# Performance work log

Measured on AMD Instinct MI355X. Metric: run time of the kernel, lower is better.

Reference implementation:

```python
import jax, jax.numpy as jnp
import numpy as np

B, T, I, H, O = 64, 2048, 128, 256, 128
K1 = 1
K2 = 1


def setup_inputs() -> dict:
    key = jax.random.key(0)
    ks = jax.random.split(key, 8)
    M = H - K1 + 1
    return {
        "x": jax.random.normal(ks[0], (B, T, I), jnp.float32),
        "W_in": jax.random.normal(ks[1], (H, I), jnp.float32) / np.sqrt(I).astype(np.float32),
        "b_in": jax.random.normal(ks[2], (H,), jnp.float32) * 0.01,
        "W_out": jax.random.normal(ks[3], (O, H), jnp.float32) / np.sqrt(H).astype(np.float32),
        "b_out": jax.random.normal(ks[4], (O,), jnp.float32) * 0.01,
        # padded Householder vectors: row i uses its first K+i entries (masked in reference)
        # uniform in [0.5, 1.5] keeps u.u well away from 0 (avoids 2/<u,u> blowup)
        "u_raw": jax.random.uniform(ks[5], (M, H), jnp.float32, 0.5, 1.5),
        "sigmas": jnp.ones((H,), jnp.float32),
        "v_raw": jax.random.uniform(ks[6], (M, H), jnp.float32, 0.5, 1.5),
    }


def _householder_chain(hats):
    # U <- H_last @ ... @ H_0, H_i = I - 2/<u,u> u u^T, applied as rank-1 updates
    Hdim = hats.shape[1]
    def step(Umat, u):
        beta = 2.0 / jnp.dot(u, u)
        return Umat - beta * jnp.outer(u, u @ Umat), None
    U, _ = jax.lax.scan(step, jnp.eye(Hdim, dtype=hats.dtype), hats)
    return U


def reference(x, W_in, b_in, W_out, b_out, u_raw, sigmas, v_raw):
    Hdim = sigmas.shape[0]
    Mu = u_raw.shape[0]
    Mv = v_raw.shape[0]
    # row i of u_hats has entries in cols [0, K1+i), then flipped along cols
    mask_u = jnp.arange(Hdim)[None, :] < (K1 + jnp.arange(Mu))[:, None]
    u_hats = jnp.flip(jnp.where(mask_u, u_raw, 0.0), axis=1)
    mask_v = jnp.arange(Hdim)[None, :] < (K2 + jnp.arange(Mv))[:, None]
    v_hats = jnp.flip(jnp.where(mask_v, v_raw, 0.0), axis=(0, 1))  # torch.flip dims=[0,1]
    U = _householder_chain(u_hats)
    V = _householder_chain(v_hats)
    W = (U * sigmas[None, :]) @ V  # U @ diag(sigmas) @ V
    # precompute input projection for all timesteps: [T, B, H]
    xproj = jnp.einsum('bti,hi->tbh', x, W_in) + b_in
    h0 = jnp.zeros((x.shape[0], Hdim), x.dtype)
    def cell(h, xp):
        h = jnp.tanh(xp + h @ W.T)
        return h, h @ W_out.T + b_out
    _, out = jax.lax.scan(cell, h0, xproj)  # out: [T, B, O]
    return jnp.transpose(out, (1, 0, 2))
```

## Files before the change

kernel.cpp:

```cpp
#include <hip/hip_runtime.h>
#include <hip/hip_bf16.h>
#include <hip/hip_fp16.h>

#define BB 64
#define TT 2048
#define II 128
#define HH 256
#define OO 128
#define RCH 8

typedef _Float16 f16x2 __attribute__((ext_vector_type(2)));
typedef _Float16 f16x8 __attribute__((ext_vector_type(8)));
typedef float f32x4 __attribute__((ext_vector_type(4)));

#if __has_builtin(__builtin_amdgcn_fdot2)
__device__ __forceinline__ float fdot2(f16x2 a, f16x2 b, float c) {
    return __builtin_amdgcn_fdot2(a, b, c, false);
}
#else
__device__ __forceinline__ float fdot2(f16x2 a, f16x2 b, float c) {
    return fmaf((float)a.x, (float)b.x, fmaf((float)a.y, (float)b.y, c));
}
#endif

__device__ __forceinline__ f16x2 u2h(unsigned int u) { return __builtin_bit_cast(f16x2, u); }
__device__ __forceinline__ unsigned int packf16(float a, float b) {
    return __builtin_bit_cast(unsigned int, f16x2{(_Float16)a, (_Float16)b});
}

__device__ __forceinline__ float tanh_fast(float x) {
    float xc = fminf(fmaxf(x, -9.0f), 9.0f);
    float e = __expf(2.0f * xc);
    return (e - 1.0f) * __fdividef(1.0f, e + 1.0f);
}

__device__ __forceinline__ void step_barrier() {
    __builtin_amdgcn_sched_barrier(0);
    asm volatile("s_waitcnt lgkmcnt(0)" ::: "memory");
    __builtin_amdgcn_s_barrier();
    __builtin_amdgcn_sched_barrier(0);
}

__global__ __launch_bounds__(64) void prep_kernel(
    const float* __restrict__ u_raw, const float* __restrict__ v_raw,
    float* __restrict__ u_eff, float* __restrict__ v_eff,
    float* __restrict__ beta_u, float* __restrict__ beta_v)
{
    const int row = blockIdx.x;
    const int lane = threadIdx.x;
    const bool isU = row < HH;
    const int i = isU ? row : row - HH;
    const float* src = isU ? (u_raw + (size_t)i * HH) : (v_raw + (size_t)(HH - 1 - i) * HH);
    float* dst = (isU ? u_eff : v_eff) + (size_t)i * HH;
    const int lo = isU ? (HH - 1 - i) : i;
    float ss = 0.0f;
    for (int c = lane; c < HH; c += 64) {
        float vv = (c >= lo) ? src[HH - 1 - c] : 0.0f;
        dst[c] = vv;
        ss += vv * vv;
    }
    for (int m = 1; m < 64; m <<= 1) ss += __shfl_xor(ss, m, 64);
    if (lane == 0) (isU ? beta_u : beta_v)[i] = 2.0f / ss;
}

__global__ __launch_bounds__(256) void hh_kernel(
    const float* __restrict__ u_eff, const float* __restrict__ v_eff,
    const float* __restrict__ beta_u, const float* __restrict__ beta_v,
    float* __restrict__ Ucol, float* __restrict__ Vrow)
{
    const int wid = blockIdx.x * 4 + (threadIdx.x >> 6);
    const int lane = threadIdx.x & 63;
    const bool isU = wid < HH;
    const int j = isU ? wid : wid - HH;
    const float* eff = isU ? u_eff : v_eff;
    const float* beta = isU ? beta_u : beta_v;

    float cr0 = (j == 4 * lane + 0) ? 1.0f : 0.0f;
    float cr1 = (j == 4 * lane + 1) ? 1.0f : 0.0f;
    float cr2 = (j == 4 * lane + 2) ? 1.0f : 0.0f;
    float cr3 = (j == 4 * lane + 3) ? 1.0f : 0.0f;

    const int i0 = isU ? (HH - 1 - j) : 0;
    for (int i = i0; i < HH; ++i) {
        const float4 v4 = *(const float4*)(eff + (size_t)i * HH + lane * 4);
        float d = v4.x * cr0 + v4.y * cr1 + v4.z * cr2 + v4.w * cr3;
        for (int m = 1; m < 64; m <<= 1) d += __shfl_xor(d, m, 64);
        const float t = beta[i] * d;
        cr0 = fmaf(-t, v4.x, cr0);
        cr1 = fmaf(-t, v4.y, cr1);
        cr2 = fmaf(-t, v4.z, cr2);
        cr3 = fmaf(-t, v4.w, cr3);
    }
    if (isU) {
        *(float4*)(Ucol + (size_t)j * HH + lane * 4) = make_float4(cr0, cr1, cr2, cr3);
    } else {
        Vrow[(size_t)(4 * lane + 0) * HH + j] = cr0;
        Vrow[(size_t)(4 * lane + 1) * HH + j] = cr1;
        Vrow[(size_t)(4 * lane + 2) * HH + j] = cr2;
        Vrow[(size_t)(4 * lane + 3) * HH + j] = cr3;
    }
}

__global__ __launch_bounds__(256) void w_kernel(
    const float* __restrict__ Ucol, const float* __restrict__ Vrow,
    const float* __restrict__ sig, float* __restrict__ Wm)
{
    const int r = blockIdx.x;
    const int c = threadIdx.x;
    float acc = 0.0f;
    #pragma unroll 4
    for (int k = 0; k < HH; ++k) {
        acc = fmaf(Ucol[(size_t)k * HH + r] * sig[k], Vrow[(size_t)k * HH + c], acc);
    }
    Wm[(size_t)r * HH + c] = acc;
}

__device__ __forceinline__ void stage16(_Float16* dst, const float* src) {
    #pragma unroll
    for (int i = 0; i < 4; ++i) {
        float4 f = ((const float4*)src)[i];
        ((f16x2*)dst)[2 * i + 0] = f16x2{(_Float16)f.x, (_Float16)f.y};
        ((f16x2*)dst)[2 * i + 1] = f16x2{(_Float16)f.z, (_Float16)f.w};
    }
}
__device__ __forceinline__ void stage16(_Float16* dst, const __half* src) {
    ((uint4*)dst)[0] = ((const uint4*)src)[0];
    ((uint4*)dst)[1] = ((const uint4*)src)[1];
}
__device__ __forceinline__ void storeC(float* p, float v) { *p = v; }
__device__ __forceinline__ void storeC(__half* p, float v) { *p = __float2half_rn(v); }

template <typename AT, typename OT>
__global__ __launch_bounds__(256) void gemm_mfma(
    const AT* __restrict__ A, const float* __restrict__ Bm,
    const float* __restrict__ bias, OT* __restrict__ C,
    int M, int N, int K)
{
    __shared__ _Float16 As[128][40];
    __shared__ _Float16 Bs[64][40];
    const int tid = threadIdx.x;
    const int m0 = blockIdx.x * 128;
    const int n0 = blockIdx.y * 64;
    const int lane = tid & 63;
    const int w = tid >> 6;
    const int lo = lane & 15;
    const int qd = lane >> 4;
    const int mh = w >> 1;
    const int nh = w & 1;
    const int srow = tid >> 1;
    const int shalf = tid & 1;

    f32x4 acc[4][2] = {};
    for (int k0 = 0; k0 < K; k0 += 32) {
        stage16(&As[srow][shalf * 16], A + (size_t)(m0 + srow) * K + k0 + shalf * 16);
        if (tid < 128)
            stage16(&Bs[srow][shalf * 16], Bm + (size_t)(n0 + srow) * K + k0 + shalf * 16);
        __syncthreads();
        f16x8 af[4], bf[2];
        #pragma unroll
        for (int mt = 0; mt < 4; ++mt)
            af[mt] = *(const f16x8*)&As[64 * mh + 16 * mt + lo][qd * 8];
        #pragma unroll
        for (int nt = 0; nt < 2; ++nt)
            bf[nt] = *(const f16x8*)&Bs[32 * nh + 16 * nt + lo][qd * 8];
        #pragma unroll
        for (int mt = 0; mt < 4; ++mt)
            #pragma unroll
            for (int nt = 0; nt < 2; ++nt)
                acc[mt][nt] = __builtin_amdgcn_mfma_f32_16x16x32_f16(
                    af[mt], bf[nt], acc[mt][nt], 0, 0, 0);
        __syncthreads();
    }
    #pragma unroll
    for (int nt = 0; nt < 2; ++nt) {
        const int n = n0 + 32 * nh + 16 * nt + lo;
        const float bv = bias[n];
        #pragma unroll
        for (int mt = 0; mt < 4; ++mt) {
            const int m = m0 + 64 * mh + 16 * mt + 4 * qd;
            #pragma unroll
            for (int r = 0; r < 4; ++r)
                storeC(C + (size_t)(m + r) * N + n, acc[mt][nt][r] + bv);
        }
    }
}

__global__ __launch_bounds__(512) void recur_kernel(
    const float* __restrict__ Wm,
    const __half* __restrict__ xp,
    __half* __restrict__ hall)
{
    const int b = blockIdx.x;
    const int tid = threadIdx.x;
    const int l = tid & 63;
    const int q = tid >> 6;
    const int lr = l & 31;
    const int kh = l >> 5;

    __shared__ __align__(16) unsigned int hbuf[2][HH / 2];

    const int row = 32 * q + lr;
    f16x2 w2[64];
    {
        const float* Wp = Wm + (size_t)row * HH + 128 * kh;
        #pragma unroll
        for (int c4 = 0; c4 < 32; ++c4) {
            float4 f = *(const float4*)(Wp + 4 * c4);
            w2[2 * c4 + 0] = f16x2{(_Float16)f.x, (_Float16)f.y};
            w2[2 * c4 + 1] = f16x2{(_Float16)f.z, (_Float16)f.w};
        }
    }
    if (tid < HH) ((unsigned int*)hbuf)[tid] = 0u;
    __syncthreads();

    const _Float16* xph = (const _Float16*)xp + (size_t)b * TT * HH + row;
    unsigned int* hw = (unsigned int*)(hall + (size_t)b * TT * HH) + 16 * q + (lr >> 1);
    const bool wr = (l < 32) && ((l & 1) == 0);

    _Float16 xpc[RCH], xpn[RCH];
    unsigned int hst[RCH];
    #pragma unroll
    for (int s = 0; s < RCH; ++s) xpc[s] = xph[(size_t)s * HH];

    int p = 0;
    const int nch = TT / RCH;
    for (int c = 0; c < nch; ++c) {
        if (c + 1 < nch) {
            const _Float16* xn = xph + (size_t)(c + 1) * RCH * HH;
            #pragma unroll
            for (int s = 0; s < RCH; ++s) xpn[s] = xn[(size_t)s * HH];
        }
        #pragma unroll
        for (int s = 0; s < RCH; ++s) {
            const uint4* hb = (const uint4*)(&hbuf[p][0]) + kh * 16;
            float a0 = 0.f, a1 = 0.f, a2 = 0.f, a3 = 0.f;
            #pragma unroll
            for (int g = 0; g < 16; ++g) {
                uint4 h4 = hb[g];
                a0 = fdot2(w2[4 * g + 0], u2h(h4.x), a0);
                a1 = fdot2(w2[4 * g + 1], u2h(h4.y), a1);
                a2 = fdot2(w2[4 * g + 2], u2h(h4.z), a2);
                a3 = fdot2(w2[4 * g + 3], u2h(h4.w), a3);
            }
            float part = (a0 + a1) + (a2 + a3);
            float tot = part + __shfl_xor(part, 32, 64);
            float hval = tanh_fast(tot + (float)xpc[s]);
            float hot = __shfl_xor(hval, 1, 64);
            unsigned int pk = packf16(hval, hot);
            hst[s] = pk;
            if (wr) hbuf[p ^ 1][16 * q + (lr >> 1)] = pk;
            step_barrier();
            p ^= 1;
        }
        if (wr) {
            unsigned int* hwc = hw + (size_t)c * RCH * 128;
            #pragma unroll
            for (int s = 0; s < RCH; ++s) hwc[(size_t)s * 128] = hst[s];
        }
        #pragma unroll
        for (int s = 0; s < RCH; ++s) xpc[s] = xpn[s];
    }
}

extern "C" void kernel_launch(void* const* d_in, const int* in_sizes, int n_in,
                              void* d_out, int out_size, void* d_ws, size_t ws_size,
                              hipStream_t stream) {
    const float* x     = (const float*)d_in[0];
    const float* W_in  = (const float*)d_in[1];
    const float* b_in  = (const float*)d_in[2];
    const float* W_out = (const float*)d_in[3];
    const float* b_out = (const float*)d_in[4];
    const float* u_raw = (const float*)d_in[5];
    const float* sig   = (const float*)d_in[6];
    const float* v_raw = (const float*)d_in[7];
    float* out = (float*)d_out;

    char* ws = (char*)d_ws;
    size_t off = 0;
    auto alloc = [&](size_t bytes) -> void* {
        void* p = (void*)(ws + off);
        off += (bytes + 255) & ~((size_t)255);
        return p;
    };
    float* u_eff  = (float*)alloc((size_t)HH * HH * 4);
    float* v_eff  = (float*)alloc((size_t)HH * HH * 4);
    float* beta_u = (float*)alloc((size_t)HH * 4);
    float* beta_v = (float*)alloc((size_t)HH * 4);
    float* Ucol   = (float*)alloc((size_t)HH * HH * 4);
    float* Vrow   = (float*)alloc((size_t)HH * HH * 4);
    float* Wm     = (float*)alloc((size_t)HH * HH * 4);
    __half* xpbuf = (__half*)alloc((size_t)BB * TT * HH * 2);
    __half* hall  = (__half*)alloc((size_t)BB * TT * HH * 2);
    (void)ws_size; (void)in_sizes; (void)n_in; (void)out_size;

    prep_kernel<<<2 * HH, 64, 0, stream>>>(u_raw, v_raw, u_eff, v_eff, beta_u, beta_v);
    hh_kernel<<<(2 * HH) / 4, 256, 0, stream>>>(u_eff, v_eff, beta_u, beta_v, Ucol, Vrow);
    w_kernel<<<HH, HH, 0, stream>>>(Ucol, Vrow, sig, Wm);
    gemm_mfma<float, __half>
        <<<dim3((BB * TT) / 128, HH / 64), 256, 0, stream>>>(x, W_in, b_in, xpbuf, BB * TT, HH, II);
    recur_kernel<<<BB, 512, 0, stream>>>(Wm, xpbuf, hall);
    gemm_mfma<__half, float>
        <<<dim3((BB * TT) / 128, OO / 64), 256, 0, stream>>>(hall, W_out, b_out, out, BB * TT, OO, HH);
}
```

Measured before the change: 1.550 ms.

## Split recurrence matvec by K across waves with readlane broadcast and LDS partial sums

The per-step h·W^T work is repartitioned so each wave owns a 32-wide K slice for all 256 output rows (4 rows per lane). The hidden-state slice is broadcast from registers with readlane instead of being read from LDS. Partial sums from the 8 waves are written to shared memory and reduced after the barrier. This removes the LDS vector reads of h, at the cost of a cross-wave partial-sum exchange and a serial readlane chain on every step.

```diff
diff --git a/kernel.cpp b/kernel.cpp
--- a/kernel.cpp
+++ b/kernel.cpp
@@ -195,33 +195,33 @@
     const int l = tid & 63;
     const int q = tid >> 6;
     const int lr = l & 31;
-    const int kh = l >> 5;
-
-    __shared__ __align__(16) unsigned int hbuf[2][HH / 2];
-
-    const int row = 32 * q + lr;
-    f16x2 w2[64];
-    {
-        const float* Wp = Wm + (size_t)row * HH + 128 * kh;
-        #pragma unroll
-        for (int c4 = 0; c4 < 32; ++c4) {
-            float4 f = *(const float4*)(Wp + 4 * c4);
-            w2[2 * c4 + 0] = f16x2{(_Float16)f.x, (_Float16)f.y};
-            w2[2 * c4 + 1] = f16x2{(_Float16)f.z, (_Float16)f.w};
-        }
-    }
-    if (tid < HH) ((unsigned int*)hbuf)[tid] = 0u;
-    __syncthreads();
-
-    const _Float16* xph = (const _Float16*)xp + (size_t)b * TT * HH + row;
-    unsigned int* hw = (unsigned int*)(hall + (size_t)b * TT * HH) + 16 * q + (lr >> 1);
-    const bool wr = (l < 32) && ((l & 1) == 0);
+    const int hh = l >> 5;
+
+    __shared__ float ps[2][8][HH];
+
+    f16x2 w2[4][16];
+    #pragma unroll
+    for (int r = 0; r < 4; ++r) {
+        const float* Wp = Wm + (size_t)(4 * l + r) * HH + q * 32;
+        #pragma unroll
+        for (int c4 = 0; c4 < 8; ++c4) {
+            float4 f = *(const float4*)(Wp + c4 * 4);
+            w2[r][c4 * 2 + 0] = f16x2{(_Float16)f.x, (_Float16)f.y};
+            w2[r][c4 * 2 + 1] = f16x2{(_Float16)f.z, (_Float16)f.w};
+        }
+    }
+
+    const int e = 32 * q + lr;
+    const _Float16* xph = (const _Float16*)xp + (size_t)b * TT * HH + e;
+    unsigned int* hw = (unsigned int*)(hall + (size_t)b * TT * HH) + (e >> 1);
+    const bool st = (l < 32) && !(l & 1);
 
     _Float16 xpc[RCH], xpn[RCH];
     unsigned int hst[RCH];
     #pragma unroll
     for (int s = 0; s < RCH; ++s) xpc[s] = xph[(size_t)s * HH];
 
+    unsigned int v = 0u;
     int p = 0;
     const int nch = TT / RCH;
     for (int c = 0; c < nch; ++c) {
@@ -232,33 +232,34 @@
         }
         #pragma unroll
         for (int s = 0; s < RCH; ++s) {
-            const uint4* hb = (const uint4*)(&hbuf[p][0]) + kh * 16;
             float a0 = 0.f, a1 = 0.f, a2 = 0.f, a3 = 0.f;
             #pragma unroll
-            for (int g = 0; g < 16; ++g) {
-                uint4 h4 = hb[g];
-                a0 = fdot2(w2[4 * g + 0], u2h(h4.x), a0);
-                a1 = fdot2(w2[4 * g + 1], u2h(h4.y), a1);
-                a2 = fdot2(w2[4 * g + 2], u2h(h4.z), a2);
-                a3 = fdot2(w2[4 * g + 3], u2h(h4.w), a3);
+            for (int j = 0; j < 16; ++j) {
+                f16x2 hj = u2h((unsigned int)__builtin_amdgcn_readlane((int)v, 2 * j));
+                a0 = fdot2(w2[0][j], hj, a0);
+                a1 = fdot2(w2[1][j], hj, a1);
+                a2 = fdot2(w2[2][j], hj, a2);
+                a3 = fdot2(w2[3][j], hj, a3);
             }
-            float part = (a0 + a1) + (a2 + a3);
-            float tot = part + __shfl_xor(part, 32, 64);
-            float hval = tanh_fast(tot + (float)xpc[s]);
-            float hot = __shfl_xor(hval, 1, 64);
-            unsigned int pk = packf16(hval, hot);
-            hst[s] = pk;
-            if (wr) hbuf[p ^ 1][16 * q + (lr >> 1)] = pk;
+            *(float4*)&ps[p][q][4 * l] = make_float4(a0, a1, a2, a3);
             step_barrier();
+
+            float s4 = (ps[p][4 * hh + 0][e] + ps[p][4 * hh + 1][e])
+                     + (ps[p][4 * hh + 2][e] + ps[p][4 * hh + 3][e]);
+            float tot = s4 + __shfl_xor(s4, 32, 64);
+            float hv = tanh_fast(tot + (float)xpc[s]);
+            float ho = __shfl_xor(hv, 1, 64);
+            v = packf16(hv, ho);
+            hst[s] = v;
             p ^= 1;
         }
-        if (wr) {
+        if (st) {
             unsigned int* hwc = hw + (size_t)c * RCH * 128;
             #pragma unroll
-            for (int s = 0; s < RCH; ++s) hwc[(size_t)s * 128] = hst[s];
-        }
-        #pragma unroll
-        for (int s = 0; s < RCH; ++s) xpc[s] = xpn[s];
+            for (int s2 = 0; s2 < RCH; ++s2) hwc[(size_t)s2 * 128] = hst[s2];
+        }
+        #pragma unroll
+        for (int s2 = 0; s2 < RCH; ++s2) xpc[s2] = xpn[s2];
     }
 }
 
```

Result: no change. 1.572 ms (+1.4%).
